# Kernel tuning notes

Measured on AMD Instinct MI355X. Metric: run time of the kernel, lower is better.

The kernel has to match this reference:

```python
import jax, jax.numpy as jnp
import numpy as np

N, L, D = 4, 4096, 1024
H = 16
HD = D // H          # 64
MLP = 4 * D          # 4096
EPS = 1e-5

def log_g(x):
    # torch: where(x>=0, log(relu(x)+0.5), -softplus(-x))
    return jnp.where(x >= 0.0, jnp.log(jax.nn.relu(x) + 0.5), -jax.nn.softplus(-x))

def parallel_scan_log(log_coeffs, log_values):
    # log_coeffs: (B, L, C); log_values: (B, L+1, C)
    a_star = jnp.pad(jnp.cumsum(log_coeffs, axis=1), ((0, 0), (1, 0), (0, 0)))
    log_h = jax.lax.cumlogsumexp(log_values - a_star, axis=1)
    return jnp.exp(a_star[:, 1:] + log_h[:, 1:])

def layer_norm(x, gamma, beta):
    mu = jnp.mean(x, axis=-1, keepdims=True)
    var = jnp.var(x, axis=-1, keepdims=True)
    return (x - mu) * jax.lax.rsqrt(var + EPS) * gamma + beta

def setup_inputs() -> dict:
    key = jax.random.key(0)
    ks = jax.random.split(key, 12)
    s = 0.02
    return {
        "x": jax.random.normal(ks[0], (N, L, D), jnp.float32),
        "h_0": jax.random.normal(ks[1], (N, 1, D), jnp.float32),
        "w_in": jax.random.normal(ks[2], (D, D), jnp.float32) * s,
        "b_in": jnp.zeros((D,), jnp.float32),
        "wz": jax.random.normal(ks[3], (HD, HD), jnp.float32) * s,
        "bz": jnp.zeros((HD,), jnp.float32),
        "wh": jax.random.normal(ks[4], (HD, HD), jnp.float32) * s,
        "bh": jnp.zeros((HD,), jnp.float32),
        "w_out": jax.random.normal(ks[5], (D, D), jnp.float32) * s,
        "b_out": jnp.zeros((D,), jnp.float32),
        "ln1_g": jnp.ones((D,), jnp.float32),
        "ln1_b": jnp.zeros((D,), jnp.float32),
        "ln2_g": jnp.ones((D,), jnp.float32),
        "ln2_b": jnp.zeros((D,), jnp.float32),
        "mw1": jax.random.normal(ks[6], (D, MLP), jnp.float32) * s,
        "mb1": jnp.zeros((MLP,), jnp.float32),
        "mw2": jax.random.normal(ks[7], (MLP, MLP), jnp.float32) * s,
        "mb2": jnp.zeros((MLP,), jnp.float32),
        "mw3": jax.random.normal(ks[8], (MLP, D), jnp.float32) * s,
        "mb3": jnp.zeros((D,), jnp.float32),
    }

def reference(x, h_0, w_in, b_in, wz, bz, wh, bh, w_out, b_out,
              ln1_g, ln1_b, ln2_g, ln2_b, mw1, mb1, mw2, mb2, mw3, mb3):
    n, l, d = x.shape
    rnn_input = layer_norm(x, ln1_g, ln1_b)
    pi = rnn_input @ w_in + b_in                                 # (N,L,D)
    pi = pi.reshape(n, l, H, HD).transpose(0, 2, 1, 3).reshape(n * H, l, HD)
    h0 = h_0.reshape(n, 1, H, HD).transpose(0, 2, 1, 3).reshape(n * H, 1, HD)
    # minGRU in log-space
    k = pi @ wz + bz
    log_z = -jax.nn.softplus(-k)
    log_coeffs = -jax.nn.softplus(k)
    log_h0 = log_g(h0)
    log_th = log_g(pi @ wh + bh)
    h = parallel_scan_log(log_coeffs, jnp.concatenate([log_h0, log_z + log_th], axis=1))
    rnn_states = h.reshape(n, H, l, HD).transpose(0, 2, 1, 3).reshape(n, l, d)
    x = x + (rnn_states @ w_out + b_out)
    mlp_in = layer_norm(x, ln2_g, ln2_b)
    y = jax.nn.silu(mlp_in @ mw1 + mb1)
    y = jax.nn.silu(y @ mw2 + mb2)
    y = y @ mw3 + mb3
    return (x + y, rnn_states)
```

## Files before the change

### kernel.cpp

```cpp
#include <hip/hip_runtime.h>
#include <hip/hip_bf16.h>

typedef __attribute__((ext_vector_type(8))) short short8;
typedef __attribute__((ext_vector_type(4))) float f32x4;
using bf16 = __hip_bfloat16;

#define DEV static __device__ __forceinline__

DEV float bf2f(bf16 v) { return __bfloat162float(v); }
DEV bf16 f2bf(float v) { return __float2bfloat16(v); }

DEV void gld_lds16(const void* g, void* l) {
  __builtin_amdgcn_global_load_lds(
      (const __attribute__((address_space(1))) void*)g,
      (__attribute__((address_space(3))) void*)l, 16, 0, 0);
}

__global__ __launch_bounds__(256)
void wconv_kernel(const float* __restrict__ w, bf16* __restrict__ wT, int K, int N) {
  __shared__ float tile[32][33];
  const int kt = blockIdx.x * 32, nt = blockIdx.y * 32;
  const int tx = threadIdx.x & 31, ty = threadIdx.x >> 5;
#pragma unroll
  for (int i = 0; i < 32; i += 8)
    tile[ty + i][tx] = w[(size_t)(kt + ty + i) * N + nt + tx];
  __syncthreads();
#pragma unroll
  for (int i = 0; i < 32; i += 8)
    wT[(size_t)(nt + ty + i) * K + kt + tx] = f2bf(tile[tx][ty + i]);
}

__global__ __launch_bounds__(256)
void ln_kernel(const float* __restrict__ x, const float* __restrict__ g,
               const float* __restrict__ b, bf16* __restrict__ out) {
  const int row = blockIdx.x;
  const int t = threadIdx.x;
  const float4 v = ((const float4*)(x + (size_t)row * 1024))[t];
  float s = v.x + v.y + v.z + v.w;
  float ss = v.x * v.x + v.y * v.y + v.z * v.z + v.w * v.w;
#pragma unroll
  for (int off = 32; off > 0; off >>= 1) {
    s += __shfl_down(s, off);
    ss += __shfl_down(ss, off);
  }
  __shared__ float red[8];
  if ((t & 63) == 0) { red[(t >> 6) * 2] = s; red[(t >> 6) * 2 + 1] = ss; }
  __syncthreads();
  s = red[0] + red[2] + red[4] + red[6];
  ss = red[1] + red[3] + red[5] + red[7];
  const float mu = s * (1.f / 1024.f);
  const float rstd = rsqrtf(ss * (1.f / 1024.f) - mu * mu + 1e-5f);
  const float4 g4 = ((const float4*)g)[t];
  const float4 b4 = ((const float4*)b)[t];
  struct alignas(8) B4 { bf16 v[4]; } o;
  o.v[0] = f2bf((v.x - mu) * rstd * g4.x + b4.x);
  o.v[1] = f2bf((v.y - mu) * rstd * g4.y + b4.y);
  o.v[2] = f2bf((v.z - mu) * rstd * g4.z + b4.z);
  o.v[3] = f2bf((v.w - mu) * rstd * g4.w + b4.w);
  *(B4*)(out + (size_t)row * 1024 + t * 4) = o;
}

template <int EPI>
__global__ __launch_bounds__(256, 2)
void gemm128(const bf16* __restrict__ A, const bf16* __restrict__ BT,
             const float* __restrict__ bias, const float* __restrict__ res,
             void* __restrict__ C, int M, int N, int K) {
  __shared__ short As[128 * 64];
  __shared__ short Bs[128 * 64];
  const int tid = threadIdx.x;
  const int l = tid & 63;
  const int w = tid >> 6;
  const int wr = w >> 1, wc = w & 1;

  const int nbn = N >> 7;
  const int nwg = gridDim.x;
  const int bid = blockIdx.x;
  const int q = nwg >> 3, r = nwg & 7;
  const int xcd = bid & 7, lin = bid >> 3;
  const int wg = (xcd < r ? xcd * (q + 1) : r * (q + 1) + (xcd - r) * q) + lin;
  const int bm = wg / nbn, bn = wg % nbn;

  const bf16* Ab = A + (size_t)bm * 128 * K;
  const bf16* Bb = BT + (size_t)bn * 128 * K;

  f32x4 acc[4][4];
#pragma unroll
  for (int i = 0; i < 4; ++i)
#pragma unroll
    for (int j = 0; j < 4; ++j) acc[i][j] = (f32x4){0.f, 0.f, 0.f, 0.f};

  const int srow = l >> 3;
  const int scol = (((l & 7) ^ (l >> 3)) << 3);

  for (int k0 = 0; k0 < K; k0 += 64) {
    __syncthreads();
#pragma unroll
    for (int p = 0; p < 4; ++p) {
      const int rowA = p * 32 + w * 8 + srow;
      gld_lds16(Ab + (size_t)rowA * K + k0 + scol, As + (p * 32 + w * 8) * 64);
      gld_lds16(Bb + (size_t)rowA * K + k0 + scol, Bs + (p * 32 + w * 8) * 64);
    }
    __syncthreads();
    const int xr = (l & 7) << 3;
#pragma unroll
    for (int kk = 0; kk < 2; ++kk) {
      short8 fa[4], fb[4];
#pragma unroll
      for (int m = 0; m < 4; ++m)
        fa[m] = *(const short8*)&As[(wr * 64 + m * 16 + (l & 15)) * 64 +
                                    ((kk * 32 + (l >> 4) * 8) ^ xr)];
#pragma unroll
      for (int n = 0; n < 4; ++n)
        fb[n] = *(const short8*)&Bs[(wc * 64 + n * 16 + (l & 15)) * 64 +
                                    ((kk * 32 + (l >> 4) * 8) ^ xr)];
#pragma unroll
      for (int m = 0; m < 4; ++m)
#pragma unroll
        for (int n = 0; n < 4; ++n)
          acc[m][n] = __builtin_amdgcn_mfma_f32_16x16x32_bf16(fa[m], fb[n], acc[m][n], 0, 0, 0);
    }
  }

  const int lc = l & 15;
  const int lr = (l >> 4) * 4;
#pragma unroll
  for (int n = 0; n < 4; ++n) {
    const int col = bn * 128 + wc * 64 + n * 16 + lc;
    const float bv = bias[col];
#pragma unroll
    for (int m = 0; m < 4; ++m) {
      const int row = bm * 128 + wr * 64 + m * 16 + lr;
#pragma unroll
      for (int r2 = 0; r2 < 4; ++r2) {
        float v = acc[m][n][r2] + bv;
        const size_t off = (size_t)(row + r2) * N + col;
        if constexpr (EPI == 1) v = v / (1.f + __expf(-v));
        if constexpr (EPI == 2) {
          ((float*)C)[off] = res[off] + v;
        } else {
          ((bf16*)C)[off] = f2bf(v);
        }
      }
    }
  }
  (void)M;
}

template <int EPI>
__global__ __launch_bounds__(512, 2)
void gemm256(const bf16* __restrict__ A, const bf16* __restrict__ BT,
             const float* __restrict__ bias, const float* __restrict__ res,
             void* __restrict__ C, int M, int N, int K) {
  __shared__ alignas(16) short As[2][256 * 64];
  __shared__ alignas(16) short Bs[2][256 * 64];
  const int tid = threadIdx.x;
  const int l = tid & 63;
  const int w = tid >> 6;
  const int wr = w >> 2;
  const int wc = w & 3;

  const int nbn = N >> 8;
  const int nwg = gridDim.x;
  const int bid = blockIdx.x;
  const int q = nwg >> 3, r = nwg & 7;
  const int xcd = bid & 7, lin = bid >> 3;
  const int wg = (xcd < r ? xcd * (q + 1) : r * (q + 1) + (xcd - r) * q) + lin;
  const int bm = wg / nbn, bn = wg % nbn;

  const bf16* Ab = A + (size_t)bm * 256 * K;
  const bf16* Bb = BT + (size_t)bn * 256 * K;

  const int gcol = ((l & 7) ^ (l >> 3)) << 3;
  const int fr = l & 15;
  const int kq = (l >> 4) << 3;
  const int xr = (l & 7) << 3;
  const int k0s = kq ^ xr;
  const int k1s = (32 + kq) ^ xr;

  const bf16* Abl = Ab + (size_t)(w * 16 + (l >> 3)) * K + gcol;
  const bf16* Bbl = Bb + (size_t)(w * 16 + (l >> 3)) * K + gcol;

  f32x4 acc[8][4];
#pragma unroll
  for (int i = 0; i < 8; ++i)
#pragma unroll
    for (int j = 0; j < 4; ++j) acc[i][j] = (f32x4){0.f, 0.f, 0.f, 0.f};

  short8 fa[2][2];
  short8 fb[4][2];

#define BARX() __builtin_amdgcn_s_barrier()
#define SBAR0() __builtin_amdgcn_sched_barrier(0)

#define STAGE_A(BUF, HALF, KT)                                                     \
  do {                                                                             \
    gld_lds16(Abl + (size_t)((HALF) * 128) * K + (size_t)(KT) * 64,                \
              &As[BUF][((HALF) * 128 + w * 16) * 64]);                             \
    gld_lds16(Abl + (size_t)((HALF) * 128 + 8) * K + (size_t)(KT) * 64,            \
              &As[BUF][((HALF) * 128 + w * 16 + 8) * 64]);                         \
  } while (0)

#define STAGE_B(BUF, HALF, KT)                                                     \
  do {                                                                             \
    gld_lds16(Bbl + (size_t)((HALF) * 128) * K + (size_t)(KT) * 64,                \
              &Bs[BUF][((HALF) * 128 + w * 16) * 64]);                             \
    gld_lds16(Bbl + (size_t)((HALF) * 128 + 8) * K + (size_t)(KT) * 64,            \
              &Bs[BUF][((HALF) * 128 + w * 16 + 8) * 64]);                         \
  } while (0)

#define RD_FA(BUF, Q)                                                                    \
  do {                                                                                  \
    fa[0][0] = *(const short8*)&As[BUF][(wr * 128 + (Q) * 32 + fr) * 64 + k0s];         \
    fa[0][1] = *(const short8*)&As[BUF][(wr * 128 + (Q) * 32 + fr) * 64 + k1s];         \
    fa[1][0] = *(const short8*)&As[BUF][(wr * 128 + (Q) * 32 + 16 + fr) * 64 + k0s];    \
    fa[1][1] = *(const short8*)&As[BUF][(wr * 128 + (Q) * 32 + 16 + fr) * 64 + k1s];    \
  } while (0)

#define RD_FB(BUF)                                                                      \
  do {                                                                                 \
    _Pragma("unroll") for (int n_ = 0; n_ < 4; ++n_) {                                 \
      fb[n_][0] = *(const short8*)&Bs[BUF][(wc * 64 + n_ * 16 + fr) * 64 + k0s];       \
      fb[n_][1] = *(const short8*)&Bs[BUF][(wc * 64 + n_ * 16 + fr) * 64 + k1s];       \
    }                                                                                  \
  } while (0)

#define MMA_Q(Q)                                                                        \
  do {                                                                                 \
    __builtin_amdgcn_s_setprio(1);                                                     \
    _Pragma("unroll") for (int n_ = 0; n_ < 4; ++n_) {                                 \
      acc[2 * (Q)][n_] = __builtin_amdgcn_mfma_f32_16x16x32_bf16(                      \
          fa[0][0], fb[n_][0], acc[2 * (Q)][n_], 0, 0, 0);                             \
      acc[2 * (Q) + 1][n_] = __builtin_amdgcn_mfma_f32_16x16x32_bf16(                  \
          fa[1][0], fb[n_][0], acc[2 * (Q) + 1][n_], 0, 0, 0);                         \
    }                                                                                  \
    _Pragma("unroll") for (int n_ = 0; n_ < 4; ++n_) {                                 \
      acc[2 * (Q)][n_] = __builtin_amdgcn_mfma_f32_16x16x32_bf16(                      \
          fa[0][1], fb[n_][1], acc[2 * (Q)][n_], 0, 0, 0);                             \
      acc[2 * (Q) + 1][n_] = __builtin_amdgcn_mfma_f32_16x16x32_bf16(                  \
          fa[1][1], fb[n_][1], acc[2 * (Q) + 1][n_], 0, 0, 0);                         \
    }                                                                                  \
    __builtin_amdgcn_s_setprio(0);                                                     \
  } while (0)

#define LGKM0() do { asm volatile("s_waitcnt lgkmcnt(0)"); SBAR0(); } while (0)

#define TILE(BUF, T, HASA, HASB)                                                       \
  do {                                                                                 \
                                                                               \
    LGKM0();                                                                           \
    MMA_Q(0);                                                                          \
    if (HASA) { STAGE_A((BUF) ^ 1, 0, (T) + 1); STAGE_A((BUF) ^ 1, 1, (T) + 1); }      \
    RD_FA(BUF, 1);                                                                     \
    SBAR0(); BARX();                                                                   \
                                                                               \
    LGKM0();                                                                           \
    MMA_Q(1);                                                                          \
    RD_FA(BUF, 2);                                                                     \
    SBAR0(); BARX();                                                                   \
                                                                               \
    LGKM0();                                                                           \
    MMA_Q(2);                                                                          \
    if (HASB) STAGE_B(BUF, 0, (T) + 2);                                                \
    if (HASA) {                                                                        \
      if (HASB) asm volatile("s_waitcnt vmcnt(2)" ::: "memory");                       \
      else      asm volatile("s_waitcnt vmcnt(0)" ::: "memory");                       \
    }                                                                                  \
    RD_FA(BUF, 3);                                                                     \
    SBAR0(); BARX();                                                                   \
                                                                               \
    LGKM0();                                                                           \
    MMA_Q(3);                                                                          \
    if (HASB) STAGE_B(BUF, 1, (T) + 2);                                                \
    if (HASA) {                                                                        \
      RD_FB((BUF) ^ 1);                                                                \
      RD_FA((BUF) ^ 1, 0);                                                             \
      SBAR0(); BARX();                                                                 \
    }                                                                                  \
  } while (0)

  STAGE_A(0, 0, 0); STAGE_A(0, 1, 0);
  STAGE_B(0, 0, 0); STAGE_B(0, 1, 0);
  STAGE_B(1, 0, 1); STAGE_B(1, 1, 1);
  asm volatile("s_waitcnt vmcnt(4)" ::: "memory");
  BARX();
  RD_FB(0);
  RD_FA(0, 0);

  const int NT = K >> 6;
  const int NI = NT >> 1;
#pragma unroll 1
  for (int i = 0; i < NI; ++i) {
    const int t0 = 2 * i;
    const bool b0 = (t0 + 2) < NT;
    const bool b1 = (t0 + 3) < NT;
    TILE(0, t0, true, b0);
    TILE(1, t0 + 1, b0, b1);
  }

#undef BARX
#undef SBAR0
#undef STAGE_A
#undef STAGE_B
#undef RD_FA
#undef RD_FB
#undef MMA_Q
#undef LGKM0
#undef TILE

  const int lc = l & 15;
  const int lr = (l >> 4) * 4;
#pragma unroll
  for (int n = 0; n < 4; ++n) {
    const int col = bn * 256 + wc * 64 + n * 16 + lc;
    const float bv = bias[col];
#pragma unroll
    for (int m = 0; m < 8; ++m) {
      const int row = bm * 256 + wr * 128 + m * 16 + lr;
#pragma unroll
      for (int r2 = 0; r2 < 4; ++r2) {
        float v = acc[m][n][r2] + bv;
        const size_t off = (size_t)(row + r2) * N + col;
        if constexpr (EPI == 1) v = v / (1.f + __expf(-v));
        if constexpr (EPI == 2) {
          ((float*)C)[off] = res[off] + v;
        } else {
          ((bf16*)C)[off] = f2bf(v);
        }
      }
    }
  }
  (void)M;
}

__global__ __launch_bounds__(256)
void heads_kernel(const bf16* __restrict__ piB,
                  const float* __restrict__ wz, const float* __restrict__ bz,
                  const float* __restrict__ wh, const float* __restrict__ bh,
                  bf16* __restrict__ aB, bf16* __restrict__ bB) {
  __shared__ float wzs[4096], whs[4096], pis[4096];
  const int h = blockIdx.y;
  const int t0 = blockIdx.x * 64;
  const int tid = threadIdx.x;
#pragma unroll
  for (int i = tid; i < 4096; i += 256) {
    wzs[i] = wz[i];
    whs[i] = wh[i];
    pis[i] = bf2f(piB[(size_t)(t0 + (i >> 6)) * 1024 + h * 64 + (i & 63)]);
  }
  __syncthreads();
  const int hd = tid & 63;
  const int tb = (tid >> 6) * 16;
  float accK[16], accT[16];
  const float bzv = bz[hd], bhv = bh[hd];
#pragma unroll
  for (int i = 0; i < 16; ++i) { accK[i] = bzv; accT[i] = bhv; }
  for (int j = 0; j < 64; ++j) {
    const float wzv = wzs[j * 64 + hd];
    const float whv = whs[j * 64 + hd];
#pragma unroll
    for (int i = 0; i < 16; ++i) {
      const float p = pis[(tb + i) * 64 + j];
      accK[i] = fmaf(p, wzv, accK[i]);
      accT[i] = fmaf(p, whv, accT[i]);
    }
  }
#pragma unroll
  for (int i = 0; i < 16; ++i) {
    const float k = accK[i], th = accT[i];
    const float sig = 1.f / (1.f + __expf(-k));
    const float a = 1.f - sig;
    const float gg = th >= 0.f ? th + 0.5f : 1.f / (1.f + __expf(-th));
    const float bb = sig * gg;
    const size_t idx = (size_t)(t0 + tb + i) * 1024 + h * 64 + hd;
    aB[idx] = f2bf(a);
    bB[idx] = f2bf(bb);
  }
}

__global__ __launch_bounds__(256)
void scan_phase1(const bf16* __restrict__ aB, const bf16* __restrict__ bB,
                 float* __restrict__ cA, float* __restrict__ cB) {
  const int idx = blockIdx.x * 256 + threadIdx.x;
  const int c = idx & 1023;
  const int chunk = (idx >> 10) & 63;
  const int n = idx >> 16;
  size_t base = ((size_t)(n * 4096 + chunk * 64)) * 1024 + c;
  float A = 1.f, B = 0.f;
#pragma unroll 8
  for (int s = 0; s < 64; ++s) {
    const float a = bf2f(aB[base]);
    const float b = bf2f(bB[base]);
    A *= a;
    B = fmaf(a, B, b);
    base += 1024;
  }
  const size_t o = ((size_t)(n * 64 + chunk)) * 1024 + c;
  cA[o] = A;
  cB[o] = B;
}

__global__ __launch_bounds__(256)
void scan_phase2(const float* __restrict__ h0,
                 const float* __restrict__ cA, const float* __restrict__ cB,
                 float* __restrict__ hst) {
  const int idx = blockIdx.x * 256 + threadIdx.x;
  const int c = idx & 1023;
  const int n = idx >> 10;
  float hv = h0[(size_t)n * 1024 + c];
  hv = hv >= 0.f ? hv + 0.5f : 1.f / (1.f + __expf(-hv));
  for (int ch = 0; ch < 64; ++ch) {
    const size_t o = ((size_t)(n * 64 + ch)) * 1024 + c;
    hst[o] = hv;
    hv = fmaf(cA[o], hv, cB[o]);
  }
}

__global__ __launch_bounds__(256)
void scan_phase3(const bf16* __restrict__ aB, const bf16* __restrict__ bB,
                 const float* __restrict__ hst,
                 float* __restrict__ rnn, bf16* __restrict__ rnnB) {
  const int idx = blockIdx.x * 256 + threadIdx.x;
  const int c = idx & 1023;
  const int chunk = (idx >> 10) & 63;
  const int n = idx >> 16;
  float hv = hst[((size_t)(n * 64 + chunk)) * 1024 + c];
  size_t base = ((size_t)(n * 4096 + chunk * 64)) * 1024 + c;
#pragma unroll 4
  for (int s = 0; s < 64; ++s) {
    const float a = bf2f(aB[base]);
    const float b = bf2f(bB[base]);
    hv = fmaf(a, hv, b);
    rnn[base] = hv;
    rnnB[base] = f2bf(hv);
    base += 1024;
  }
}

extern "C" void kernel_launch(void* const* d_in, const int* in_sizes, int n_in,
                              void* d_out, int out_size, void* d_ws, size_t ws_size,
                              hipStream_t stream) {
  const float* x    = (const float*)d_in[0];
  const float* h0   = (const float*)d_in[1];
  const float* w_in = (const float*)d_in[2];
  const float* b_in = (const float*)d_in[3];
  const float* wz   = (const float*)d_in[4];
  const float* bz   = (const float*)d_in[5];
  const float* wh   = (const float*)d_in[6];
  const float* bh   = (const float*)d_in[7];
  const float* w_out= (const float*)d_in[8];
  const float* b_out= (const float*)d_in[9];
  const float* ln1g = (const float*)d_in[10];
  const float* ln1b = (const float*)d_in[11];
  const float* ln2g = (const float*)d_in[12];
  const float* ln2b = (const float*)d_in[13];
  const float* mw1  = (const float*)d_in[14];
  const float* mb1  = (const float*)d_in[15];
  const float* mw2  = (const float*)d_in[16];
  const float* mb2  = (const float*)d_in[17];
  const float* mw3  = (const float*)d_in[18];
  const float* mb3  = (const float*)d_in[19];
  (void)in_sizes; (void)n_in; (void)out_size;

  float* out0 = (float*)d_out;
  float* out1 = (float*)d_out + (size_t)16384 * 1024;

  char* ws = (char*)d_ws;
  size_t o = 0;
  auto take = [&](size_t bytes) { char* p = ws + o; o += (bytes + 255) & ~(size_t)255; return p; };
  bf16* w_inT = (bf16*)take((size_t)1024 * 1024 * 2);
  bf16* w_outT= (bf16*)take((size_t)1024 * 1024 * 2);
  bf16* mw1T  = (bf16*)take((size_t)4096 * 1024 * 2);
  bf16* mw2T  = (bf16*)take((size_t)4096 * 4096 * 2);
  bf16* mw3T  = (bf16*)take((size_t)4096 * 1024 * 2);
  bf16* lnxB  = (bf16*)take((size_t)16384 * 1024 * 2);
  bf16* piB   = (bf16*)take((size_t)16384 * 1024 * 2);
  bf16* aB    = (bf16*)take((size_t)16384 * 1024 * 2);
  bf16* bB    = (bf16*)take((size_t)16384 * 1024 * 2);
  float* cA   = (float*)take((size_t)4 * 64 * 1024 * 4);
  float* cB   = (float*)take((size_t)4 * 64 * 1024 * 4);
  float* hst  = (float*)take((size_t)4 * 64 * 1024 * 4);
  if (o > ws_size) return;

  wconv_kernel<<<dim3(32, 32), 256, 0, stream>>>(w_in, w_inT, 1024, 1024);
  wconv_kernel<<<dim3(32, 32), 256, 0, stream>>>(w_out, w_outT, 1024, 1024);
  wconv_kernel<<<dim3(32, 128), 256, 0, stream>>>(mw1, mw1T, 1024, 4096);
  wconv_kernel<<<dim3(128, 128), 256, 0, stream>>>(mw2, mw2T, 4096, 4096);
  wconv_kernel<<<dim3(128, 32), 256, 0, stream>>>(mw3, mw3T, 4096, 1024);

  ln_kernel<<<16384, 256, 0, stream>>>(x, ln1g, ln1b, lnxB);
  gemm256<0><<<256, 512, 0, stream>>>(lnxB, w_inT, b_in, nullptr, piB, 16384, 1024, 1024);

  heads_kernel<<<dim3(256, 16), 256, 0, stream>>>(piB, wz, bz, wh, bh, aB, bB);
  scan_phase1<<<1024, 256, 0, stream>>>(aB, bB, cA, cB);
  scan_phase2<<<16, 256, 0, stream>>>(h0, cA, cB, hst);
  scan_phase3<<<1024, 256, 0, stream>>>(aB, bB, hst, out1, lnxB );

  gemm256<2><<<256, 512, 0, stream>>>(lnxB, w_outT, b_out, x, out0, 16384, 1024, 1024);

  ln_kernel<<<16384, 256, 0, stream>>>(out0, ln2g, ln2b, lnxB );
  bf16* t1 = aB;
  bf16* t2 = bB;
  for (int mc = 0; mc < 4; ++mc) {
    const bf16* a3 = lnxB + (size_t)mc * 4096 * 1024;
    gemm256<1><<<256, 512, 0, stream>>>(a3, mw1T, mb1, nullptr, t1, 4096, 4096, 1024);
    gemm256<1><<<256, 512, 0, stream>>>(t1, mw2T, mb2, nullptr, t2, 4096, 4096, 4096);
    float* oc = out0 + (size_t)mc * 4096 * 1024;
    gemm128<2><<<256, 256, 0, stream>>>(t2, mw3T, mb3, oc, oc, 4096, 1024, 4096);
  }
}
```

Measured before the change: 1.376 ms.

## Fuse scan phase1 into heads kernel and vectorize scan phase3

The heads kernel now computes per-chunk scan products (A, B) in registers and reduces them across its four warps in shared memory. This removes the separate scan_phase1 pass, which re-read aB and bB. scan_phase3 now handles 8 channels per thread with 16-byte bf16 loads and float4 stores, and the pi tile load in the heads kernel is vectorized. The GEMM epilogues are reordered to be row-major with the bias reloaded per element, which may add extra loads and register pressure. Phase3 now launches only 256 blocks of 128 threads, so less parallelism is available to hide memory latency.

```diff
diff --git a/kernel.cpp b/kernel.cpp
--- a/kernel.cpp
+++ b/kernel.cpp
@@ -2,6 +2,7 @@
 #include <hip/hip_bf16.h>
 
 typedef __attribute__((ext_vector_type(8))) short short8;
+typedef __attribute__((ext_vector_type(4))) short short4v;
 typedef __attribute__((ext_vector_type(4))) float f32x4;
 using bf16 = __hip_bfloat16;
 
@@ -9,6 +10,15 @@
 
 DEV float bf2f(bf16 v) { return __bfloat162float(v); }
 DEV bf16 f2bf(float v) { return __float2bfloat16(v); }
+DEV float s2f(short s) {
+  union { unsigned u; float f; } v;
+  v.u = ((unsigned)(unsigned short)s) << 16;
+  return v.f;
+}
+DEV short f2s(float v) {
+  bf16 b = __float2bfloat16(v);
+  return *(short*)&b;
+}
 
 DEV void gld_lds16(const void* g, void* l) {
   __builtin_amdgcn_global_load_lds(
@@ -123,17 +133,20 @@
 
   const int lc = l & 15;
   const int lr = (l >> 4) * 4;
-#pragma unroll
-  for (int n = 0; n < 4; ++n) {
-    const int col = bn * 128 + wc * 64 + n * 16 + lc;
-    const float bv = bias[col];
-#pragma unroll
-    for (int m = 0; m < 4; ++m) {
-      const int row = bm * 128 + wr * 64 + m * 16 + lr;
-#pragma unroll
-      for (int r2 = 0; r2 < 4; ++r2) {
-        float v = acc[m][n][r2] + bv;
-        const size_t off = (size_t)(row + r2) * N + col;
+  float bv4[2];
+#pragma unroll
+  for (int n = 0; n < 2; ++n) bv4[n] = 0.f;
+#pragma unroll
+  for (int m = 0; m < 4; ++m) {
+    const int row = bm * 128 + wr * 64 + m * 16 + lr;
+#pragma unroll
+    for (int r2 = 0; r2 < 4; ++r2) {
+      const size_t rowoff = (size_t)(row + r2) * N;
+#pragma unroll
+      for (int n = 0; n < 4; ++n) {
+        const int col = bn * 128 + wc * 64 + n * 16 + lc;
+        float v = acc[m][n][r2] + bias[col];
+        const size_t off = rowoff + col;
         if constexpr (EPI == 1) v = v / (1.f + __expf(-v));
         if constexpr (EPI == 2) {
           ((float*)C)[off] = res[off] + v;
@@ -143,7 +156,7 @@
       }
     }
   }
-  (void)M;
+  (void)M; (void)bv4;
 }
 
 template <int EPI>
@@ -310,16 +323,16 @@
   const int lc = l & 15;
   const int lr = (l >> 4) * 4;
 #pragma unroll
-  for (int n = 0; n < 4; ++n) {
-    const int col = bn * 256 + wc * 64 + n * 16 + lc;
-    const float bv = bias[col];
-#pragma unroll
-    for (int m = 0; m < 8; ++m) {
-      const int row = bm * 256 + wr * 128 + m * 16 + lr;
-#pragma unroll
-      for (int r2 = 0; r2 < 4; ++r2) {
-        float v = acc[m][n][r2] + bv;
-        const size_t off = (size_t)(row + r2) * N + col;
+  for (int m = 0; m < 8; ++m) {
+    const int row = bm * 256 + wr * 128 + m * 16 + lr;
+#pragma unroll
+    for (int r2 = 0; r2 < 4; ++r2) {
+      const size_t rowoff = (size_t)(row + r2) * N;
+#pragma unroll
+      for (int n = 0; n < 4; ++n) {
+        const int col = bn * 256 + wc * 64 + n * 16 + lc;
+        float v = acc[m][n][r2] + bias[col];
+        const size_t off = rowoff + col;
         if constexpr (EPI == 1) v = v / (1.f + __expf(-v));
         if constexpr (EPI == 2) {
           ((float*)C)[off] = res[off] + v;
@@ -336,8 +349,10 @@
 void heads_kernel(const bf16* __restrict__ piB,
                   const float* __restrict__ wz, const float* __restrict__ bz,
                   const float* __restrict__ wh, const float* __restrict__ bh,
-                  bf16* __restrict__ aB, bf16* __restrict__ bB) {
+                  bf16* __restrict__ aB, bf16* __restrict__ bB,
+                  float* __restrict__ cA, float* __restrict__ cB) {
   __shared__ float wzs[4096], whs[4096], pis[4096];
+  __shared__ float segA[4][64], segB[4][64];
   const int h = blockIdx.y;
   const int t0 = blockIdx.x * 64;
   const int tid = threadIdx.x;
@@ -345,7 +360,16 @@
   for (int i = tid; i < 4096; i += 256) {
     wzs[i] = wz[i];
     whs[i] = wh[i];
-    pis[i] = bf2f(piB[(size_t)(t0 + (i >> 6)) * 1024 + h * 64 + (i & 63)]);
+  }
+#pragma unroll
+  for (int rr = 0; rr < 4; ++rr) {
+    const int v = tid + rr * 256;
+    const int row = v >> 4, c4 = (v & 15) * 4;
+    short4v p4 = *(const short4v*)(piB + (size_t)(t0 + row) * 1024 + h * 64 + c4);
+    pis[row * 64 + c4 + 0] = s2f(p4[0]);
+    pis[row * 64 + c4 + 1] = s2f(p4[1]);
+    pis[row * 64 + c4 + 2] = s2f(p4[2]);
+    pis[row * 64 + c4 + 3] = s2f(p4[3]);
   }
   __syncthreads();
   const int hd = tid & 63;
@@ -364,6 +388,7 @@
       accT[i] = fmaf(p, whv, accT[i]);
     }
   }
+  float As = 1.f, Bs = 0.f;
 #pragma unroll
   for (int i = 0; i < 16; ++i) {
     const float k = accK[i], th = accT[i];
@@ -371,32 +396,28 @@
     const float a = 1.f - sig;
     const float gg = th >= 0.f ? th + 0.5f : 1.f / (1.f + __expf(-th));
     const float bb = sig * gg;
+    Bs = fmaf(a, Bs, bb);
+    As *= a;
     const size_t idx = (size_t)(t0 + tb + i) * 1024 + h * 64 + hd;
     aB[idx] = f2bf(a);
     bB[idx] = f2bf(bb);
   }
-}
-
-__global__ __launch_bounds__(256)
-void scan_phase1(const bf16* __restrict__ aB, const bf16* __restrict__ bB,
-                 float* __restrict__ cA, float* __restrict__ cB) {
-  const int idx = blockIdx.x * 256 + threadIdx.x;
-  const int c = idx & 1023;
-  const int chunk = (idx >> 10) & 63;
-  const int n = idx >> 16;
-  size_t base = ((size_t)(n * 4096 + chunk * 64)) * 1024 + c;
-  float A = 1.f, B = 0.f;
-#pragma unroll 8
-  for (int s = 0; s < 64; ++s) {
-    const float a = bf2f(aB[base]);
-    const float b = bf2f(bB[base]);
-    A *= a;
-    B = fmaf(a, B, b);
-    base += 1024;
-  }
-  const size_t o = ((size_t)(n * 64 + chunk)) * 1024 + c;
-  cA[o] = A;
-  cB[o] = B;
+  segA[tid >> 6][hd] = As;
+  segB[tid >> 6][hd] = Bs;
+  __syncthreads();
+  if (tid < 64) {
+    float A = segA[0][tid], B = segB[0][tid];
+#pragma unroll
+    for (int s = 1; s < 4; ++s) {
+      B = fmaf(segA[s][tid], B, segB[s][tid]);
+      A *= segA[s][tid];
+    }
+    const int n = t0 >> 12;
+    const int chunk = (t0 >> 6) & 63;
+    const size_t o = ((size_t)(n * 64 + chunk)) * 1024 + h * 64 + tid;
+    cA[o] = A;
+    cB[o] = B;
+  }
 }
 
 __global__ __launch_bounds__(256)
@@ -415,23 +436,37 @@
   }
 }
 
-__global__ __launch_bounds__(256)
+__global__ __launch_bounds__(128)
 void scan_phase3(const bf16* __restrict__ aB, const bf16* __restrict__ bB,
                  const float* __restrict__ hst,
                  float* __restrict__ rnn, bf16* __restrict__ rnnB) {
-  const int idx = blockIdx.x * 256 + threadIdx.x;
-  const int c = idx & 1023;
-  const int chunk = (idx >> 10) & 63;
-  const int n = idx >> 16;
-  float hv = hst[((size_t)(n * 64 + chunk)) * 1024 + c];
-  size_t base = ((size_t)(n * 4096 + chunk * 64)) * 1024 + c;
+  const int idx = blockIdx.x * 128 + threadIdx.x;
+  const int c8 = idx & 127;
+  const int chunk = (idx >> 7) & 63;
+  const int n = idx >> 13;
+  const int c0 = c8 * 8;
+  float hv[8];
+  const float4* hsrc = (const float4*)(hst + ((size_t)(n * 64 + chunk)) * 1024 + c0);
+  float4 ha = hsrc[0], hb = hsrc[1];
+  hv[0] = ha.x; hv[1] = ha.y; hv[2] = ha.z; hv[3] = ha.w;
+  hv[4] = hb.x; hv[5] = hb.y; hv[6] = hb.z; hv[7] = hb.w;
+  size_t base = ((size_t)(n * 4096 + chunk * 64)) * 1024 + c0;
 #pragma unroll 4
   for (int s = 0; s < 64; ++s) {
-    const float a = bf2f(aB[base]);
-    const float b = bf2f(bB[base]);
-    hv = fmaf(a, hv, b);
-    rnn[base] = hv;
-    rnnB[base] = f2bf(hv);
+    const short8 a8 = *(const short8*)(aB + base);
+    const short8 b8 = *(const short8*)(bB + base);
+    short8 ob;
+    float4 o0, o1;
+#pragma unroll
+    for (int j = 0; j < 8; ++j) {
+      hv[j] = fmaf(s2f(a8[j]), hv[j], s2f(b8[j]));
+      ob[j] = f2s(hv[j]);
+    }
+    o0.x = hv[0]; o0.y = hv[1]; o0.z = hv[2]; o0.w = hv[3];
+    o1.x = hv[4]; o1.y = hv[5]; o1.z = hv[6]; o1.w = hv[7];
+    ((float4*)(rnn + base))[0] = o0;
+    ((float4*)(rnn + base))[1] = o1;
+    *(short8*)(rnnB + base) = ob;
     base += 1024;
   }
 }
@@ -490,10 +525,9 @@
   ln_kernel<<<16384, 256, 0, stream>>>(x, ln1g, ln1b, lnxB);
   gemm256<0><<<256, 512, 0, stream>>>(lnxB, w_inT, b_in, nullptr, piB, 16384, 1024, 1024);
 
-  heads_kernel<<<dim3(256, 16), 256, 0, stream>>>(piB, wz, bz, wh, bh, aB, bB);
-  scan_phase1<<<1024, 256, 0, stream>>>(aB, bB, cA, cB);
+  heads_kernel<<<dim3(256, 16), 256, 0, stream>>>(piB, wz, bz, wh, bh, aB, bB, cA, cB);
   scan_phase2<<<16, 256, 0, stream>>>(h0, cA, cB, hst);
-  scan_phase3<<<1024, 256, 0, stream>>>(aB, bB, hst, out1, lnxB );
+  scan_phase3<<<256, 128, 0, stream>>>(aB, bB, hst, out1, lnxB );
 
   gemm256<2><<<256, 512, 0, stream>>>(lnxB, w_outT, b_out, x, out0, 16384, 1024, 1024);
 
```

After: 1.294 ms. 6.0% less time.
